# Kernel optimization log

Measured on AMD Instinct MI355X. Metric: run time of the kernel, lower is better.

## Reference

```python
import jax, jax.numpy as jnp
import numpy as np

NUM_HEADS = 16
NEG_FILL = -10000.0  # matches torch masked_fill value in source


def setup_inputs() -> dict:
    key = jax.random.key(0)
    ks = jax.random.split(key, 8)
    B, S, H = 4, 2048, 1024
    sc = 1.0 / np.sqrt(H)
    x = jax.random.normal(ks[0], (B, S, H), dtype=jnp.float32)
    L = jax.random.randint(ks[1], (B,), 1, S + 1, dtype=jnp.int64 if jax.config.jax_enable_x64 else jnp.int32)
    Wq = jax.random.normal(ks[2], (H, H), dtype=jnp.float32) * sc
    Wk = jax.random.normal(ks[3], (H, H), dtype=jnp.float32) * sc
    Wv = jax.random.normal(ks[4], (H, H), dtype=jnp.float32) * sc
    bv = jax.random.normal(ks[5], (H,), dtype=jnp.float32) * 0.01
    Wo = jax.random.normal(ks[6], (H, H), dtype=jnp.float32) * sc
    bo = jax.random.normal(ks[7], (H,), dtype=jnp.float32) * 0.01
    return {"x": x, "L": L, "Wq": Wq, "Wk": Wk, "Wv": Wv, "bv": bv, "Wo": Wo, "bo": bo}


def reference(x, L, Wq, Wk, Wv, bv, Wo, bo):
    # AttentionAggregator.forward with L given; dropout in eval mode (identity).
    B, S, H = x.shape
    nh = NUM_HEADS
    dk = H // nh
    # torch nn.Linear: y = x @ W.T + b
    q = (x @ Wq.T).reshape(B, S, nh, dk).transpose(0, 2, 1, 3)  # (B,h,S,dk)
    k = (x @ Wk.T).reshape(B, S, nh, dk).transpose(0, 2, 1, 3)
    v = (x @ Wv.T + bv).reshape(B, S, nh, dk).transpose(0, 2, 1, 3)
    scores = jnp.einsum("bhqd,bhkd->bhqk", q, k) / jnp.sqrt(jnp.float32(dk))
    valid = jnp.arange(S)[None, :] < L[:, None]  # (B,S) True where real token
    scores = jnp.where(valid[:, None, None, :], scores, NEG_FILL)
    attn = jax.nn.softmax(scores, axis=-1)
    ctx = jnp.einsum("bhqk,bhkd->bhqd", attn, v)
    ctx = ctx.transpose(0, 2, 1, 3).reshape(B, S, H)
    attn_out = ctx @ Wo.T + bo  # (B,S,H)
    # masked mean pool over valid positions
    m = valid.astype(x.dtype)  # (B,S)
    pooled = jnp.einsum("bsh,bs->bh", attn_out, m) / m.sum(axis=1, keepdims=True)
    return pooled
```

## Files before the change

### kernel.cpp

```cpp
#include <hip/hip_runtime.h>
#include <hip/hip_bf16.h>
#include <math.h>

constexpr int Bc = 4, Sc = 2048, Hc = 1024, NHc = 16, DKc = 64;

constexpr size_t XHOFF = 0;
constexpr size_t QOFF  = 4194304;
constexpr size_t KOFF  = 8388608;
constexpr size_t WQOFF = 12582912;
constexpr size_t WKOFF = 13107200;
constexpr size_t LIOFF = 13631488;
constexpr size_t WOFF  = 13762560;
constexpr size_t YOFF  = 13893632;
constexpr size_t CSOFF = 13959168;
constexpr size_t YPOFF = 13963264;

typedef __attribute__((ext_vector_type(8))) short bf16x8;
typedef __attribute__((ext_vector_type(4))) float f32x4;

__device__ inline short f2bf(float v) {
    __hip_bfloat16 h = __float2bfloat16(v);
    return *reinterpret_cast<short*>(&h);
}

__device__ inline float ex2(float x) {
#if defined(__has_builtin) && __has_builtin(__builtin_amdgcn_exp2f)
    return __builtin_amdgcn_exp2f(x);
#else
    float r; asm("v_exp_f32 %0, %1" : "=v"(r) : "v"(x)); return r;
#endif
}

__device__ inline void gld_lds16(const void* g, void* l) {
    __builtin_amdgcn_global_load_lds(
        (const __attribute__((address_space(1))) unsigned int*)g,
        (__attribute__((address_space(3))) unsigned int*)l, 16, 0, 0);
}

__global__ __launch_bounds__(256) void cvt_all_kernel(
    const float* __restrict__ x, const float* __restrict__ Wq,
    const float* __restrict__ Wk, float* __restrict__ ws)
{
    const size_t i = ((size_t)blockIdx.x * 256 + threadIdx.x) * 8;
    const float* src; short* dst; float scale; size_t off;
    constexpr float QSC = 0.125f * 1.44269504088896340736f;
    if (i < 8388608)       { src = x;  dst = (short*)(ws + XHOFF); off = i;            scale = 1.0f; }
    else if (i < 9437184)  { src = Wq; dst = (short*)(ws + WQOFF); off = i - 8388608;  scale = QSC;  }
    else                   { src = Wk; dst = (short*)(ws + WKOFF); off = i - 9437184;  scale = 1.0f; }
    float4 a = *(const float4*)(src + off);
    float4 b = *(const float4*)(src + off + 4);
    bf16x8 o;
    o[0] = f2bf(a.x * scale); o[1] = f2bf(a.y * scale);
    o[2] = f2bf(a.z * scale); o[3] = f2bf(a.w * scale);
    o[4] = f2bf(b.x * scale); o[5] = f2bf(b.y * scale);
    o[6] = f2bf(b.z * scale); o[7] = f2bf(b.w * scale);
    *(bf16x8*)(dst + off) = o;
}

__global__ __launch_bounds__(256) void proj_mfma_kernel(
    const int* __restrict__ L, float* __restrict__ ws)
{
    const int z  = blockIdx.z;
    const int m0 = blockIdx.y * 128;
    const int n0 = blockIdx.x * 128;
    const int b  = m0 >> 11;
    const int s0 = m0 & 2047;
    const int Lb = L[b];
    if (s0 >= Lb) return;

    const short* __restrict__ A = (const short*)(ws + XHOFF);
    const short* __restrict__ W = (const short*)(ws + (z == 0 ? WQOFF : WKOFF));
    short* __restrict__ Out = (short*)(ws + (z == 0 ? QOFF : KOFF));

    __shared__ __align__(16) short As[128 * 32];
    __shared__ __align__(16) short Bs[128 * 32];

    const int tid  = threadIdx.x;
    const int lane = tid & 63;
    const int wave = tid >> 6;
    const int l16  = lane & 15, quad = lane >> 4;
    const int wm = (wave & 1) * 64, wn = (wave >> 1) * 64;

    const int c0 = tid, c1 = tid + 256;
    const int r0 = c0 >> 2, g0 = (c0 & 3) * 8;
    const int r1 = c1 >> 2, g1 = (c1 & 3) * 8;
    short* lA0 = As + wave * 512;
    short* lA1 = As + 2048 + wave * 512;
    short* lB0 = Bs + wave * 512;
    short* lB1 = Bs + 2048 + wave * 512;

    const f32x4 z4 = {0.f, 0.f, 0.f, 0.f};
    f32x4 acc[4][4];
    #pragma unroll
    for (int i = 0; i < 4; ++i)
        #pragma unroll
        for (int j = 0; j < 4; ++j) acc[i][j] = z4;

    for (int k0 = 0; k0 < Hc; k0 += 32) {
        __syncthreads();
        gld_lds16(A + (size_t)(m0 + r0) * Hc + k0 + g0, lA0);
        gld_lds16(A + (size_t)(m0 + r1) * Hc + k0 + g1, lA1);
        gld_lds16(W + (size_t)(n0 + r0) * Hc + k0 + g0, lB0);
        gld_lds16(W + (size_t)(n0 + r1) * Hc + k0 + g1, lB1);
        __syncthreads();

        bf16x8 af[4], bfr[4];
        #pragma unroll
        for (int mt = 0; mt < 4; ++mt)
            af[mt] = *(const bf16x8*)(As + (wm + mt * 16 + l16) * 32 + quad * 8);
        #pragma unroll
        for (int nt = 0; nt < 4; ++nt)
            bfr[nt] = *(const bf16x8*)(Bs + (wn + nt * 16 + l16) * 32 + quad * 8);
        #pragma unroll
        for (int mt = 0; mt < 4; ++mt)
            #pragma unroll
            for (int nt = 0; nt < 4; ++nt)
                acc[mt][nt] = __builtin_amdgcn_mfma_f32_16x16x32_bf16(
                    af[mt], bfr[nt], acc[mt][nt], 0, 0, 0);
    }

    #pragma unroll
    for (int mt = 0; mt < 4; ++mt) {
        #pragma unroll
        for (int nt = 0; nt < 4; ++nt) {
            const int n = n0 + wn + nt * 16 + l16;
            const int h = n >> 6, d = n & 63;
            #pragma unroll
            for (int r = 0; r < 4; ++r) {
                const int s = s0 + wm + mt * 16 + quad * 4 + r;
                Out[(((size_t)b * NHc + h) * Sc + s) * DKc + d] =
                    f2bf(acc[mt][nt][r]);
            }
        }
    }
}

__global__ __launch_bounds__(256) void rowsum_kernel(
    const int* __restrict__ L, float* __restrict__ ws)
{
    const int bh = blockIdx.x;
    const int qs = blockIdx.y;
    const int b  = bh >> 4;
    const int Lb = L[b];
    if (qs * 256 >= Lb) return;

    const int tid  = threadIdx.x;
    const int wave = tid >> 6;
    const int lane = tid & 63;
    const int l16 = lane & 15, quad = lane >> 4;
    const int q0 = qs * 256 + wave * 64;

    const short* __restrict__ qarr = (const short*)(ws + QOFF) + (size_t)bh * Sc * DKc;
    const short* __restrict__ karr = (const short*)(ws + KOFF) + (size_t)bh * Sc * DKc;

    __shared__ __align__(16) short Ks[4][3][32 * 64];

    const int srow = lane >> 3;
    const int scol = (lane & 7) ^ srow;
    const short* ksrc = karr + (size_t)srow * DKc + scol * 8;

    bf16x8 bq[4][2];
    #pragma unroll
    for (int g = 0; g < 4; ++g) {
        const short* qr = qarr + (size_t)(q0 + g * 16 + l16) * DKc;
        bq[g][0] = *(const bf16x8*)(qr + quad * 8);
        bq[g][1] = *(const bf16x8*)(qr + 32 + quad * 8);
    }
    float lacc[4] = {0.f, 0.f, 0.f, 0.f};

    const int n = (Lb + 31) >> 5;

    auto stage = [&](int s, int kt) {
        short* dst = &Ks[wave][s][0];
        #pragma unroll
        for (int j = 0; j < 4; ++j)
            gld_lds16(ksrc + (size_t)(kt + j * 8) * DKc, dst + j * 512);
    };

    stage(0, 0);
    if (n > 1) stage(1, 32);
    if (n > 2) stage(2, 64);

    int slot = 0;
    for (int t = 0; t < n; ++t) {
        const int kt = t << 5;
        if (t + 2 < n)      asm volatile("s_waitcnt vmcnt(8)" ::: "memory");
        else if (t + 1 < n) asm volatile("s_waitcnt vmcnt(4)" ::: "memory");
        else                asm volatile("s_waitcnt vmcnt(0)" ::: "memory");

        const short* B = &Ks[wave][slot][0];
        if (kt + 32 <= Lb) {
            #pragma unroll
            for (int tt = 0; tt < 2; ++tt) {
                const int r = tt * 16 + l16;
                const bf16x8 alo = *(const bf16x8*)(B + r * 64 + (quad ^ (r & 7)) * 8);
                const bf16x8 ahi = *(const bf16x8*)(B + r * 64 + ((4 + quad) ^ (r & 7)) * 8);
                #pragma unroll
                for (int g = 0; g < 4; ++g) {
                    f32x4 c = {0.f, 0.f, 0.f, 0.f};
                    c = __builtin_amdgcn_mfma_f32_16x16x32_bf16(alo, bq[g][0], c, 0, 0, 0);
                    c = __builtin_amdgcn_mfma_f32_16x16x32_bf16(ahi, bq[g][1], c, 0, 0, 0);
                    lacc[g] += (ex2(c[0]) + ex2(c[1])) + (ex2(c[2]) + ex2(c[3]));
                }
            }
        } else {
            #pragma unroll
            for (int tt = 0; tt < 2; ++tt) {
                const int r = tt * 16 + l16;
                const bf16x8 alo = *(const bf16x8*)(B + r * 64 + (quad ^ (r & 7)) * 8);
                const bf16x8 ahi = *(const bf16x8*)(B + r * 64 + ((4 + quad) ^ (r & 7)) * 8);
                #pragma unroll
                for (int g = 0; g < 4; ++g) {
                    f32x4 c = {0.f, 0.f, 0.f, 0.f};
                    c = __builtin_amdgcn_mfma_f32_16x16x32_bf16(alo, bq[g][0], c, 0, 0, 0);
                    c = __builtin_amdgcn_mfma_f32_16x16x32_bf16(ahi, bq[g][1], c, 0, 0, 0);
                    #pragma unroll
                    for (int rr = 0; rr < 4; ++rr) {
                        const bool kv = (kt + tt * 16 + quad * 4 + rr) < Lb;
                        lacc[g] += kv ? ex2(c[rr]) : 0.f;
                    }
                }
            }
        }
        if (t + 3 < n) stage(slot, kt + 96);
        slot = (slot == 2) ? 0 : slot + 1;
    }

    #pragma unroll
    for (int g = 0; g < 4; ++g) {
        lacc[g] += __shfl_xor(lacc[g], 16, 64);
        lacc[g] += __shfl_xor(lacc[g], 32, 64);
    }
    float* __restrict__ li = ws + LIOFF + (size_t)bh * Sc;
    #pragma unroll
    for (int g = 0; g < 4; ++g)
        if (quad == g) li[q0 + g * 16 + l16] = 1.0f / lacc[g];
}

__global__ __launch_bounds__(256) void colsum_kernel(
    const int* __restrict__ L, float* __restrict__ ws)
{
    const int bh = blockIdx.x;
    const int ks = blockIdx.y;
    const int b  = bh >> 4;
    const int Lb = L[b];
    if (ks * 256 >= Lb) return;

    const int tid  = threadIdx.x;
    const int wave = tid >> 6;
    const int lane = tid & 63;
    const int l16 = lane & 15, quad = lane >> 4;
    const int k0 = ks * 256 + wave * 64;

    const short* __restrict__ qarr = (const short*)(ws + QOFF) + (size_t)bh * Sc * DKc;
    const short* __restrict__ karr = (const short*)(ws + KOFF) + (size_t)bh * Sc * DKc;
    const float* __restrict__ liarr = ws + LIOFF + (size_t)bh * Sc;

    __shared__ __align__(16) short Qs[4][3][32 * 64];
    __shared__ __align__(16) float Lis[2048];

    bf16x8 ak[4][2];
    #pragma unroll
    for (int g = 0; g < 4; ++g) {
        const short* kr = karr + (size_t)(k0 + g * 16 + l16) * DKc;
        ak[g][0] = *(const bf16x8*)(kr + quad * 8);
        ak[g][1] = *(const bf16x8*)(kr + 32 + quad * 8);
    }

    #pragma unroll
    for (int j2 = 0; j2 < 2; ++j2)
        gld_lds16(liarr + wave * 512 + j2 * 256 + lane * 4,
                  &Lis[wave * 512 + j2 * 256]);
    __syncthreads();

    const int srow = lane >> 3;
    const int scol = (lane & 7) ^ srow;
    const short* qsrc = qarr + (size_t)srow * DKc + scol * 8;

    f32x4 w[4];
    #pragma unroll
    for (int g = 0; g < 4; ++g) w[g] = (f32x4){0.f, 0.f, 0.f, 0.f};

    const int n = (Lb + 31) >> 5;

    auto stage = [&](int s, int qt) {
        short* dst = &Qs[wave][s][0];
        #pragma unroll
        for (int j = 0; j < 4; ++j)
            gld_lds16(qsrc + (size_t)(qt + j * 8) * DKc, dst + j * 512);
    };

    stage(0, 0);
    if (n > 1) stage(1, 32);
    if (n > 2) stage(2, 64);

    int slot = 0;
    for (int t = 0; t < n; ++t) {
        const int qt = t << 5;
        if (t + 2 < n)      asm volatile("s_waitcnt vmcnt(8)" ::: "memory");
        else if (t + 1 < n) asm volatile("s_waitcnt vmcnt(4)" ::: "memory");
        else                asm volatile("s_waitcnt vmcnt(0)" ::: "memory");

        const short* B = &Qs[wave][slot][0];
        const bool full = (qt + 32 <= Lb);
        #pragma unroll
        for (int tt = 0; tt < 2; ++tt) {
            const int r = tt * 16 + l16;
            const bf16x8 blo = *(const bf16x8*)(B + r * 64 + (quad ^ (r & 7)) * 8);
            const bf16x8 bhi = *(const bf16x8*)(B + r * 64 + ((4 + quad) ^ (r & 7)) * 8);
            const float lv = (full || qt + r < Lb) ? Lis[qt + r] : 0.f;
            #pragma unroll
            for (int g = 0; g < 4; ++g) {
                f32x4 c = {0.f, 0.f, 0.f, 0.f};
                c = __builtin_amdgcn_mfma_f32_16x16x32_bf16(ak[g][0], blo, c, 0, 0, 0);
                c = __builtin_amdgcn_mfma_f32_16x16x32_bf16(ak[g][1], bhi, c, 0, 0, 0);
                #pragma unroll
                for (int rr = 0; rr < 4; ++rr)
                    w[g][rr] += ex2(c[rr]) * lv;
            }
        }
        if (t + 3 < n) stage(slot, qt + 96);
        slot = (slot == 2) ? 0 : slot + 1;
    }

    #pragma unroll
    for (int off = 1; off <= 8; off <<= 1)
        #pragma unroll
        for (int g = 0; g < 4; ++g)
            #pragma unroll
            for (int rr = 0; rr < 4; ++rr)
                w[g][rr] += __shfl_xor(w[g][rr], off, 64);
    if (l16 == 0) {
        float* __restrict__ warr = ws + WOFF + (size_t)bh * Sc;
        #pragma unroll
        for (int g = 0; g < 4; ++g)
            #pragma unroll
            for (int rr = 0; rr < 4; ++rr)
                warr[k0 + g * 16 + quad * 4 + rr] = w[g][rr];
    }
}

__global__ __launch_bounds__(256) void yw_part_kernel(
    const float* __restrict__ x, const int* __restrict__ L,
    float* __restrict__ ws)
{
    const int b  = blockIdx.y;
    const int j0 = blockIdx.x * 64;
    const int s0 = blockIdx.z * 128;
    const int Lb = L[b];
    if (s0 >= Lb) return;
    const int js = threadIdx.x & 63;
    const int sl = threadIdx.x >> 6;
    const float* __restrict__ warr = ws + WOFF + (size_t)b * NHc * Sc;
    const float* __restrict__ xb = x + (size_t)b * Sc * Hc;

    __shared__ float wt[128][20];
    __shared__ float red[4][16][64];

    #pragma unroll
    for (int i = 0; i < 8; ++i) {
        const int s = (threadIdx.x & 15) + 16 * i;
        const int h = threadIdx.x >> 4;
        float v = 0.f;
        if (s0 + s < Lb) v = warr[(size_t)h * Sc + s0 + s];
        wt[s][h] = v;
    }
    __syncthreads();

    float acc[16];
    #pragma unroll
    for (int h = 0; h < 16; ++h) acc[h] = 0.f;

    #pragma unroll 4
    for (int s = sl; s < 128; s += 4) {
        const float xv = xb[(size_t)(s0 + s) * Hc + j0 + js];
        const f32x4 wa = *(const f32x4*)&wt[s][0];
        const f32x4 wb = *(const f32x4*)&wt[s][4];
        const f32x4 wc = *(const f32x4*)&wt[s][8];
        const f32x4 wd = *(const f32x4*)&wt[s][12];
        #pragma unroll
        for (int h = 0; h < 4; ++h) acc[h]      += wa[h] * xv;
        #pragma unroll
        for (int h = 0; h < 4; ++h) acc[4 + h]  += wb[h] * xv;
        #pragma unroll
        for (int h = 0; h < 4; ++h) acc[8 + h]  += wc[h] * xv;
        #pragma unroll
        for (int h = 0; h < 4; ++h) acc[12 + h] += wd[h] * xv;
    }
    #pragma unroll
    for (int h = 0; h < 16; ++h) red[sl][h][js] = acc[h];
    __syncthreads();
    if (sl == 0) {
        float* __restrict__ yp = ws + YPOFF +
            ((size_t)blockIdx.z * Bc * NHc + (size_t)b * NHc) * Hc;
        #pragma unroll
        for (int h = 0; h < 16; ++h)
            yp[(size_t)h * Hc + j0 + js] =
                red[0][h][js] + red[1][h][js] + red[2][h][js] + red[3][h][js];
    }
}

__global__ __launch_bounds__(256) void yw_reduce_kernel(
    const int* __restrict__ L, float* __restrict__ ws)
{
    const int b = blockIdx.y;
    const int i = blockIdx.x * 256 + threadIdx.x;
    const int nc = (L[b] + 127) >> 7;
    const float* __restrict__ p = ws + YPOFF + (size_t)b * NHc * Hc + i;
    float acc = 0.f;
    for (int c = 0; c < nc; ++c)
        acc += p[(size_t)c * Bc * NHc * Hc];
    ws[YOFF + (size_t)b * NHc * Hc + i] = acc;
}

__global__ __launch_bounds__(256) void csum_kernel(
    const float* __restrict__ Wv, const float* __restrict__ bv,
    const int* __restrict__ L, float* __restrict__ ws)
{
    const int b = blockIdx.y;
    const int h = blockIdx.x;
    const int n0 = h * 64;
    const int lane = threadIdx.x & 63;
    const int wave = threadIdx.x >> 6;
    const float Lb = (float)L[b];

    __shared__ float ys[1024];
    const float* __restrict__ y = ws + YOFF + ((size_t)b * NHc + h) * Hc;
    for (int i = threadIdx.x; i < 1024; i += 256) ys[i] = y[i];
    __syncthreads();

    f32x4 yv[4];
    #pragma unroll
    for (int p = 0; p < 4; ++p) yv[p] = *(const f32x4*)&ys[p * 256 + lane * 4];

    #pragma unroll
    for (int r = 0; r < 16; ++r) {
        const int n = n0 + wave * 16 + r;
        const float* wrow = Wv + (size_t)n * Hc;
        float a = 0.f;
        #pragma unroll
        for (int p = 0; p < 4; ++p) {
            const f32x4 wv = *(const f32x4*)(wrow + p * 256 + lane * 4);
            a += wv[0]*yv[p][0] + wv[1]*yv[p][1] + wv[2]*yv[p][2] + wv[3]*yv[p][3];
        }
        #pragma unroll
        for (int off = 32; off > 0; off >>= 1) a += __shfl_xor(a, off, 64);
        if (lane == 0)
            ws[CSOFF + (size_t)b * Hc + n] = a + bv[n] * Lb;
    }
}

__global__ __launch_bounds__(256) void out_kernel(
    const float* __restrict__ Wo, const float* __restrict__ bo,
    const int* __restrict__ L, const float* __restrict__ ws,
    float* __restrict__ out)
{
    const int b = blockIdx.y;
    const int o0 = blockIdx.x * 64;
    const int lane = threadIdx.x & 63;
    const int wave = threadIdx.x >> 6;
    const float linv = 1.0f / (float)L[b];

    __shared__ float cs[1024];
    const float* __restrict__ c = ws + CSOFF + (size_t)b * Hc;
    for (int i = threadIdx.x; i < 1024; i += 256) cs[i] = c[i];
    __syncthreads();

    f32x4 cv[4];
    #pragma unroll
    for (int p = 0; p < 4; ++p) cv[p] = *(const f32x4*)&cs[p * 256 + lane * 4];

    #pragma unroll
    for (int r = 0; r < 16; ++r) {
        const int o = o0 + wave * 16 + r;
        const float* wrow = Wo + (size_t)o * Hc;
        float a = 0.f;
        #pragma unroll
        for (int p = 0; p < 4; ++p) {
            const f32x4 wv = *(const f32x4*)(wrow + p * 256 + lane * 4);
            a += wv[0]*cv[p][0] + wv[1]*cv[p][1] + wv[2]*cv[p][2] + wv[3]*cv[p][3];
        }
        #pragma unroll
        for (int off = 32; off > 0; off >>= 1) a += __shfl_xor(a, off, 64);
        if (lane == 0)
            out[(size_t)b * Hc + o] = a * linv + bo[o];
    }
}

extern "C" void kernel_launch(void* const* d_in, const int* in_sizes, int n_in,
                              void* d_out, int out_size, void* d_ws, size_t ws_size,
                              hipStream_t stream)
{
    (void)in_sizes; (void)n_in; (void)out_size; (void)ws_size;
    const float* x  = (const float*)d_in[0];
    const int*   L  = (const int*)d_in[1];
    const float* Wq = (const float*)d_in[2];
    const float* Wk = (const float*)d_in[3];
    const float* Wv = (const float*)d_in[4];
    const float* bv = (const float*)d_in[5];
    const float* Wo = (const float*)d_in[6];
    const float* bo = (const float*)d_in[7];
    float* out = (float*)d_out;
    float* ws  = (float*)d_ws;

    cvt_all_kernel<<<5120, 256, 0, stream>>>(x, Wq, Wk, ws);

    dim3 gp(Hc / 128, (Bc * Sc) / 128, 2);
    proj_mfma_kernel<<<gp, 256, 0, stream>>>(L, ws);

    dim3 gr(Bc * NHc, Sc / 256);
    rowsum_kernel<<<gr, 256, 0, stream>>>(L, ws);
    colsum_kernel<<<gr, 256, 0, stream>>>(L, ws);

    dim3 gy(Hc / 64, Bc, Sc / 128);
    yw_part_kernel<<<gy, 256, 0, stream>>>(x, L, ws);

    dim3 gyr((NHc * Hc) / 256, Bc);
    yw_reduce_kernel<<<gyr, 256, 0, stream>>>(L, ws);

    dim3 gc(NHc, Bc);
    csum_kernel<<<gc, 256, 0, stream>>>(Wv, bv, L, ws);

    dim3 go(Hc / 64, Bc);
    out_kernel<<<go, 256, 0, stream>>>(Wo, bo, L, ws, out);
}
```

Measured before the change: 261.8 us.

## Split rowsum/colsum over key/query chunks with partial-sum reduce kernels

The row-sum and column-sum attention passes are restructured so that each block handles 32 rows, and each of its four waves covers a separate 512-long slice of the opposite sequence dimension. Partial sums go to a scratch region and are combined by two new small reduce kernels. The aim is to create many more independent blocks and balance the work across variable-length batches, instead of long serial loops per wave. In exchange, each loaded tile is reused by fewer rows, the LDS pipeline drops from triple to double buffering, and the extra launches add partial-sum traffic.

Measured after the change: 246.3 us. -5.9%, faster.

```diff
diff --git a/kernel.cpp b/kernel.cpp
--- a/kernel.cpp
+++ b/kernel.cpp
@@ -14,6 +14,8 @@
 constexpr size_t YOFF  = 13893632;
 constexpr size_t CSOFF = 13959168;
 constexpr size_t YPOFF = 13963264;
+constexpr size_t RPOFF = 13963264;
+constexpr size_t CPOFF = 13963264;
 
 typedef __attribute__((ext_vector_type(8))) short bf16x8;
 typedef __attribute__((ext_vector_type(4))) float f32x4;
@@ -135,68 +137,69 @@
     }
 }
 
-__global__ __launch_bounds__(256) void rowsum_kernel(
+__global__ __launch_bounds__(256) void rowsum_part_kernel(
     const int* __restrict__ L, float* __restrict__ ws)
 {
     const int bh = blockIdx.x;
-    const int qs = blockIdx.y;
+    const int qg = blockIdx.y;
     const int b  = bh >> 4;
     const int Lb = L[b];
-    if (qs * 256 >= Lb) return;
-
-    const int tid  = threadIdx.x;
-    const int wave = tid >> 6;
-    const int lane = tid & 63;
+    const int q0 = qg * 32;
+    if (q0 >= Lb) return;
+
+    const int wave = threadIdx.x >> 6;
+    const int lane = threadIdx.x & 63;
     const int l16 = lane & 15, quad = lane >> 4;
-    const int q0 = qs * 256 + wave * 64;
+
+    const int kc0 = wave * 512;
+    if (kc0 >= Lb) return;
+    const int kend = (kc0 + 512 < Lb) ? kc0 + 512 : Lb;
 
     const short* __restrict__ qarr = (const short*)(ws + QOFF) + (size_t)bh * Sc * DKc;
     const short* __restrict__ karr = (const short*)(ws + KOFF) + (size_t)bh * Sc * DKc;
 
-    __shared__ __align__(16) short Ks[4][3][32 * 64];
+    __shared__ __align__(16) short Ks[4][2][32 * 64];
 
     const int srow = lane >> 3;
     const int scol = (lane & 7) ^ srow;
-    const short* ksrc = karr + (size_t)srow * DKc + scol * 8;
-
-    bf16x8 bq[4][2];
-    #pragma unroll
-    for (int g = 0; g < 4; ++g) {
+    const short* ksrc = karr + (size_t)(kc0 + srow) * DKc + scol * 8;
+
+    bf16x8 bq[2][2];
+    #pragma unroll
+    for (int g = 0; g < 2; ++g) {
         const short* qr = qarr + (size_t)(q0 + g * 16 + l16) * DKc;
         bq[g][0] = *(const bf16x8*)(qr + quad * 8);
         bq[g][1] = *(const bf16x8*)(qr + 32 + quad * 8);
     }
-    float lacc[4] = {0.f, 0.f, 0.f, 0.f};
-
-    const int n = (Lb + 31) >> 5;
-
-    auto stage = [&](int s, int kt) {
+    float lacc[2] = {0.f, 0.f};
+
+    const int n = (kend - kc0 + 31) >> 5;
+
+    auto stage = [&](int s, int ktr) {
         short* dst = &Ks[wave][s][0];
         #pragma unroll
         for (int j = 0; j < 4; ++j)
-            gld_lds16(ksrc + (size_t)(kt + j * 8) * DKc, dst + j * 512);
+            gld_lds16(ksrc + (size_t)(ktr + j * 8) * DKc, dst + j * 512);
     };
 
     stage(0, 0);
     if (n > 1) stage(1, 32);
-    if (n > 2) stage(2, 64);
-
-    int slot = 0;
+
     for (int t = 0; t < n; ++t) {
-        const int kt = t << 5;
-        if (t + 2 < n)      asm volatile("s_waitcnt vmcnt(8)" ::: "memory");
-        else if (t + 1 < n) asm volatile("s_waitcnt vmcnt(4)" ::: "memory");
-        else                asm volatile("s_waitcnt vmcnt(0)" ::: "memory");
-
-        const short* B = &Ks[wave][slot][0];
-        if (kt + 32 <= Lb) {
+        const int ktr = t << 5;
+        const int kabs = kc0 + ktr;
+        if (t + 1 < n) asm volatile("s_waitcnt vmcnt(4)" ::: "memory");
+        else           asm volatile("s_waitcnt vmcnt(0)" ::: "memory");
+
+        const short* B = &Ks[wave][t & 1][0];
+        if (kabs + 32 <= Lb) {
             #pragma unroll
             for (int tt = 0; tt < 2; ++tt) {
                 const int r = tt * 16 + l16;
                 const bf16x8 alo = *(const bf16x8*)(B + r * 64 + (quad ^ (r & 7)) * 8);
                 const bf16x8 ahi = *(const bf16x8*)(B + r * 64 + ((4 + quad) ^ (r & 7)) * 8);
                 #pragma unroll
-                for (int g = 0; g < 4; ++g) {
+                for (int g = 0; g < 2; ++g) {
                     f32x4 c = {0.f, 0.f, 0.f, 0.f};
                     c = __builtin_amdgcn_mfma_f32_16x16x32_bf16(alo, bq[g][0], c, 0, 0, 0);
                     c = __builtin_amdgcn_mfma_f32_16x16x32_bf16(ahi, bq[g][1], c, 0, 0, 0);
@@ -210,58 +213,71 @@
                 const bf16x8 alo = *(const bf16x8*)(B + r * 64 + (quad ^ (r & 7)) * 8);
                 const bf16x8 ahi = *(const bf16x8*)(B + r * 64 + ((4 + quad) ^ (r & 7)) * 8);
                 #pragma unroll
-                for (int g = 0; g < 4; ++g) {
+                for (int g = 0; g < 2; ++g) {
                     f32x4 c = {0.f, 0.f, 0.f, 0.f};
                     c = __builtin_amdgcn_mfma_f32_16x16x32_bf16(alo, bq[g][0], c, 0, 0, 0);
                     c = __builtin_amdgcn_mfma_f32_16x16x32_bf16(ahi, bq[g][1], c, 0, 0, 0);
                     #pragma unroll
                     for (int rr = 0; rr < 4; ++rr) {
-                        const bool kv = (kt + tt * 16 + quad * 4 + rr) < Lb;
+                        const bool kv = (kabs + tt * 16 + quad * 4 + rr) < Lb;
                         lacc[g] += kv ? ex2(c[rr]) : 0.f;
                     }
                 }
             }
         }
-        if (t + 3 < n) stage(slot, kt + 96);
-        slot = (slot == 2) ? 0 : slot + 1;
-    }
-
-    #pragma unroll
-    for (int g = 0; g < 4; ++g) {
+        if (t + 2 < n) stage(t & 1, ktr + 64);
+    }
+
+    #pragma unroll
+    for (int g = 0; g < 2; ++g) {
         lacc[g] += __shfl_xor(lacc[g], 16, 64);
         lacc[g] += __shfl_xor(lacc[g], 32, 64);
     }
-    float* __restrict__ li = ws + LIOFF + (size_t)bh * Sc;
-    #pragma unroll
-    for (int g = 0; g < 4; ++g)
-        if (quad == g) li[q0 + g * 16 + l16] = 1.0f / lacc[g];
-}
-
-__global__ __launch_bounds__(256) void colsum_kernel(
+    float* __restrict__ rp = ws + RPOFF + ((size_t)wave * 64 + bh) * Sc;
+    if (quad == 0) rp[q0 + l16]      = lacc[0];
+    if (quad == 1) rp[q0 + 16 + l16] = lacc[1];
+}
+
+__global__ __launch_bounds__(256) void rowsum_reduce_kernel(
+    const int* __restrict__ L, float* __restrict__ ws)
+{
+    const int bh = blockIdx.y;
+    const int q  = blockIdx.x * 256 + threadIdx.x;
+    const int nc = (L[bh >> 4] + 511) >> 9;
+    float acc = 0.f;
+    for (int c = 0; c < nc; ++c)
+        acc += ws[RPOFF + ((size_t)c * 64 + bh) * Sc + q];
+    ws[LIOFF + (size_t)bh * Sc + q] = 1.0f / acc;
+}
+
+__global__ __launch_bounds__(256) void colsum_part_kernel(
     const int* __restrict__ L, float* __restrict__ ws)
 {
     const int bh = blockIdx.x;
-    const int ks = blockIdx.y;
+    const int kg = blockIdx.y;
     const int b  = bh >> 4;
     const int Lb = L[b];
-    if (ks * 256 >= Lb) return;
-
-    const int tid  = threadIdx.x;
-    const int wave = tid >> 6;
-    const int lane = tid & 63;
+    const int k0 = kg * 32;
+    if (k0 >= Lb) return;
+
+    const int wave = threadIdx.x >> 6;
+    const int lane = threadIdx.x & 63;
     const int l16 = lane & 15, quad = lane >> 4;
-    const int k0 = ks * 256 + wave * 64;
+
+    const int qc0 = wave * 512;
+    if (qc0 >= Lb) return;
+    const int qend = (qc0 + 512 < Lb) ? qc0 + 512 : Lb;
 
     const short* __restrict__ qarr = (const short*)(ws + QOFF) + (size_t)bh * Sc * DKc;
     const short* __restrict__ karr = (const short*)(ws + KOFF) + (size_t)bh * Sc * DKc;
     const float* __restrict__ liarr = ws + LIOFF + (size_t)bh * Sc;
 
-    __shared__ __align__(16) short Qs[4][3][32 * 64];
-    __shared__ __align__(16) float Lis[2048];
-
-    bf16x8 ak[4][2];
-    #pragma unroll
-    for (int g = 0; g < 4; ++g) {
+    __shared__ __align__(16) short Qs[4][2][32 * 64];
+    __shared__ __align__(16) float Lis[4][512];
+
+    bf16x8 ak[2][2];
+    #pragma unroll
+    for (int g = 0; g < 2; ++g) {
         const short* kr = karr + (size_t)(k0 + g * 16 + l16) * DKc;
         ak[g][0] = *(const bf16x8*)(kr + quad * 8);
         ak[g][1] = *(const bf16x8*)(kr + 32 + quad * 8);
@@ -269,48 +285,42 @@
 
     #pragma unroll
     for (int j2 = 0; j2 < 2; ++j2)
-        gld_lds16(liarr + wave * 512 + j2 * 256 + lane * 4,
-                  &Lis[wave * 512 + j2 * 256]);
-    __syncthreads();
+        gld_lds16(liarr + qc0 + j2 * 256 + lane * 4, &Lis[wave][j2 * 256]);
 
     const int srow = lane >> 3;
     const int scol = (lane & 7) ^ srow;
-    const short* qsrc = qarr + (size_t)srow * DKc + scol * 8;
-
-    f32x4 w[4];
-    #pragma unroll
-    for (int g = 0; g < 4; ++g) w[g] = (f32x4){0.f, 0.f, 0.f, 0.f};
-
-    const int n = (Lb + 31) >> 5;
-
-    auto stage = [&](int s, int qt) {
+    const short* qsrc = qarr + (size_t)(qc0 + srow) * DKc + scol * 8;
+
+    f32x4 w[2];
+    w[0] = (f32x4){0.f, 0.f, 0.f, 0.f};
+    w[1] = (f32x4){0.f, 0.f, 0.f, 0.f};
+
+    const int n = (qend - qc0 + 31) >> 5;
+
+    auto stage = [&](int s, int qtr) {
         short* dst = &Qs[wave][s][0];
         #pragma unroll
         for (int j = 0; j < 4; ++j)
-            gld_lds16(qsrc + (size_t)(qt + j * 8) * DKc, dst + j * 512);
+            gld_lds16(qsrc + (size_t)(qtr + j * 8) * DKc, dst + j * 512);
     };
 
     stage(0, 0);
     if (n > 1) stage(1, 32);
-    if (n > 2) stage(2, 64);
-
-    int slot = 0;
+
     for (int t = 0; t < n; ++t) {
-        const int qt = t << 5;
-        if (t + 2 < n)      asm volatile("s_waitcnt vmcnt(8)" ::: "memory");
-        else if (t + 1 < n) asm volatile("s_waitcnt vmcnt(4)" ::: "memory");
-        else                asm volatile("s_waitcnt vmcnt(0)" ::: "memory");
-
-        const short* B = &Qs[wave][slot][0];
-        const bool full = (qt + 32 <= Lb);
+        const int qtr = t << 5;
+        if (t + 1 < n) asm volatile("s_waitcnt vmcnt(4)" ::: "memory");
+        else           asm volatile("s_waitcnt vmcnt(0)" ::: "memory");
+
+        const short* B = &Qs[wave][t & 1][0];
         #pragma unroll
         for (int tt = 0; tt < 2; ++tt) {
             const int r = tt * 16 + l16;
             const bf16x8 blo = *(const bf16x8*)(B + r * 64 + (quad ^ (r & 7)) * 8);
             const bf16x8 bhi = *(const bf16x8*)(B + r * 64 + ((4 + quad) ^ (r & 7)) * 8);
-            const float lv = (full || qt + r < Lb) ? Lis[qt + r] : 0.f;
-            #pragma unroll
-            for (int g = 0; g < 4; ++g) {
+            const float lv = (qc0 + qtr + r < qend) ? Lis[wave][qtr + r] : 0.f;
+            #pragma unroll
+            for (int g = 0; g < 2; ++g) {
                 f32x4 c = {0.f, 0.f, 0.f, 0.f};
                 c = __builtin_amdgcn_mfma_f32_16x16x32_bf16(ak[g][0], blo, c, 0, 0, 0);
                 c = __builtin_amdgcn_mfma_f32_16x16x32_bf16(ak[g][1], bhi, c, 0, 0, 0);
@@ -319,25 +329,36 @@
                     w[g][rr] += ex2(c[rr]) * lv;
             }
         }
-        if (t + 3 < n) stage(slot, qt + 96);
-        slot = (slot == 2) ? 0 : slot + 1;
+        if (t + 2 < n) stage(t & 1, qtr + 64);
     }
 
     #pragma unroll
     for (int off = 1; off <= 8; off <<= 1)
         #pragma unroll
-        for (int g = 0; g < 4; ++g)
+        for (int g = 0; g < 2; ++g)
             #pragma unroll
             for (int rr = 0; rr < 4; ++rr)
                 w[g][rr] += __shfl_xor(w[g][rr], off, 64);
     if (l16 == 0) {
-        float* __restrict__ warr = ws + WOFF + (size_t)bh * Sc;
-        #pragma unroll
-        for (int g = 0; g < 4; ++g)
+        float* __restrict__ cp = ws + CPOFF + ((size_t)wave * 64 + bh) * Sc;
+        #pragma unroll
+        for (int g = 0; g < 2; ++g)
             #pragma unroll
             for (int rr = 0; rr < 4; ++rr)
-                warr[k0 + g * 16 + quad * 4 + rr] = w[g][rr];
-    }
+                cp[k0 + g * 16 + quad * 4 + rr] = w[g][rr];
+    }
+}
+
+__global__ __launch_bounds__(256) void colsum_reduce_kernel(
+    const int* __restrict__ L, float* __restrict__ ws)
+{
+    const int bh = blockIdx.y;
+    const int k  = blockIdx.x * 256 + threadIdx.x;
+    const int nc = (L[bh >> 4] + 511) >> 9;
+    float acc = 0.f;
+    for (int c = 0; c < nc; ++c)
+        acc += ws[CPOFF + ((size_t)c * 64 + bh) * Sc + k];
+    ws[WOFF + (size_t)bh * Sc + k] = acc;
 }
 
 __global__ __launch_bounds__(256) void yw_part_kernel(
@@ -508,9 +529,13 @@
     dim3 gp(Hc / 128, (Bc * Sc) / 128, 2);
     proj_mfma_kernel<<<gp, 256, 0, stream>>>(L, ws);
 
-    dim3 gr(Bc * NHc, Sc / 256);
-    rowsum_kernel<<<gr, 256, 0, stream>>>(L, ws);
-    colsum_kernel<<<gr, 256, 0, stream>>>(L, ws);
+    dim3 gr(Bc * NHc, Sc / 32);
+    rowsum_part_kernel<<<gr, 256, 0, stream>>>(L, ws);
+    dim3 grr(Sc / 256, Bc * NHc);
+    rowsum_reduce_kernel<<<grr, 256, 0, stream>>>(L, ws);
+
+    colsum_part_kernel<<<gr, 256, 0, stream>>>(L, ws);
+    colsum_reduce_kernel<<<grr, 256, 0, stream>>>(L, ws);
 
     dim3 gy(Hc / 64, Bc, Sc / 128);
     yw_part_kernel<<<gy, 256, 0, stream>>>(x, L, ws);
```
